# Kernel tuning notes

Hardware: AMD Instinct MI355X
Metric: run time of the kernel (lower is better)

The kernel has to match this reference:

```python
import jax, jax.numpy as jnp
import numpy as np

D = 1024
H = 16
DH = D // H


def setup_inputs() -> dict:
    key = jax.random.key(0)
    ks = jax.random.split(key, 9)
    s = 1.0 / np.sqrt(D)
    return {
        "x": jax.random.normal(ks[0], (4, 2048, D), dtype=jnp.float32),
        "wq": jax.random.uniform(ks[1], (D, D), jnp.float32, -s, s),
        "bq": jax.random.uniform(ks[2], (D,), jnp.float32, -s, s),
        "wk": jax.random.uniform(ks[3], (D, D), jnp.float32, -s, s),
        "bk": jax.random.uniform(ks[4], (D,), jnp.float32, -s, s),
        "wv": jax.random.uniform(ks[5], (D, D), jnp.float32, -s, s),
        "bv": jax.random.uniform(ks[6], (D,), jnp.float32, -s, s),
        "wo": jax.random.uniform(ks[7], (D, D), jnp.float32, -s, s),
        "bo": jax.random.uniform(ks[8], (D,), jnp.float32, -s, s),
    }


def reference(x, wq, bq, wk, bk, wv, bv, wo, bo):
    B, S, _ = x.shape
    # projections + split heads: [B, S, D] -> [B, H, S, Dh]
    def split(t):
        return t.reshape(B, S, H, DH).transpose(0, 2, 1, 3)
    q = split(x @ wq + bq)
    k = split(x @ wk + bk)
    v = split(x @ wv + bv)
    scale = 1.0 / jnp.sqrt(jnp.float32(DH))
    scores = jnp.einsum("bhqd,bhkd->bhqk", q, k) * scale  # [B,H,S,S]
    att = jax.nn.softmax(scores, axis=-1)
    out = jnp.einsum("bhqk,bhkd->bhqd", att, v)  # [B,H,S,Dh]
    out = out.transpose(0, 2, 1, 3).reshape(B, S, D)
    return out @ wo + bo
```

## Files before the change

kernel.cpp:

```cpp
#include <hip/hip_runtime.h>
#include <stdint.h>

typedef float f32x4 __attribute__((ext_vector_type(4)));
typedef __bf16 bf16x8 __attribute__((ext_vector_type(8)));
typedef unsigned short ushort_t;
typedef ushort_t ushortx8 __attribute__((ext_vector_type(8)));
typedef ushort_t ushortx4 __attribute__((ext_vector_type(4)));

#define DEV static __device__ __forceinline__

DEV ushort_t f2bf(float f) {
  union { float f; uint32_t u; } v; v.f = f;
  uint32_t u = v.u;
  return (ushort_t)((u + 0x7FFFu + ((u >> 16) & 1u)) >> 16);
}

DEV uint32_t pkbf(float a, float b) {
  __bf16 x = (__bf16)a, y = (__bf16)b;
  return (uint32_t)__builtin_bit_cast(unsigned short, x) |
         ((uint32_t)__builtin_bit_cast(unsigned short, y) << 16);
}

DEV void cp16(const void* g, void* l) {
  __builtin_amdgcn_global_load_lds((const __attribute__((address_space(1))) unsigned int*)g,
                                   (__attribute__((address_space(3))) unsigned int*)l,
                                   16, 0, 0);
}

DEV f32x4 mfma16(bf16x8 a, bf16x8 b, f32x4 c) {
  return __builtin_amdgcn_mfma_f32_16x16x32_bf16(a, b, c, 0, 0, 0);
}

__global__ __launch_bounds__(256) void k_prep(
    const float* __restrict__ x, ushort_t* __restrict__ xb,
    const float* __restrict__ wq, const float* __restrict__ wk,
    const float* __restrict__ wv, const float* __restrict__ wo,
    ushort_t* __restrict__ wqkvT, ushort_t* __restrict__ woT) {
  __shared__ float tile[32][33];
  int b = blockIdx.x;
  if (b < 4096) {
    size_t idx = ((size_t)b * 256 + threadIdx.x) * 8;
    const float4* src = (const float4*)(x + idx);
    float4 a = src[0], c = src[1];
    ushortx8 o;
    o[0] = f2bf(a.x); o[1] = f2bf(a.y); o[2] = f2bf(a.z); o[3] = f2bf(a.w);
    o[4] = f2bf(c.x); o[5] = f2bf(c.y); o[6] = f2bf(c.z); o[7] = f2bf(c.w);
    *(ushortx8*)(xb + idx) = o;
  } else {
    int t = b - 4096;
    int which = t >> 10;
    const float* src = (which == 0) ? wq : (which == 1) ? wk : (which == 2) ? wv : wo;
    ushort_t* dst = (which == 0) ? wqkvT
                    : (which == 1) ? wqkvT + 1024 * 1024
                    : (which == 2) ? wqkvT + 2 * 1024 * 1024
                                   : woT;
    int tt = t & 1023;
    int c0 = (tt & 31) * 32, r0 = (tt >> 5) * 32;
    int tx = threadIdx.x & 31, ty = threadIdx.x >> 5;
#pragma unroll
    for (int i = ty; i < 32; i += 8)
      tile[i][tx] = src[(size_t)(r0 + i) * 1024 + c0 + tx];
    __syncthreads();
#pragma unroll
    for (int i = ty; i < 32; i += 8)
      dst[(size_t)(c0 + i) * 1024 + r0 + tx] = f2bf(tile[tx][i]);
  }
}

__global__ __launch_bounds__(512, 2) void k_gemm256(
    const ushort_t* __restrict__ A, const ushort_t* __restrict__ Bt,
    const float* __restrict__ b0, const float* __restrict__ b1,
    const float* __restrict__ b2, ushort_t* __restrict__ qw,
    ushort_t* __restrict__ kw, ushort_t* __restrict__ vtw) {
  extern __shared__ ushort_t lds[];
  ushort_t* As = lds;
  ushort_t* Bs = lds + 32768;
  const int K = 1024, NT = 16;
  int tid = threadIdx.x;
  int w = tid >> 6, lane = tid & 63, l16 = lane & 15, lg = lane >> 4;
  int wr = w >> 2, wc = w & 3;
  int m0 = blockIdx.x * 256, n0 = blockIdx.y * 256;

  const ushort_t* Asrc = A + (size_t)(m0 + w * 8 + (lane >> 3)) * K +
                         (size_t)(((lane & 7) ^ (lane >> 3)) * 8);
  const ushort_t* Bsrc = Bt + (size_t)(n0 + w * 8 + (lane >> 3)) * K +
                         (size_t)(((lane & 7) ^ (lane >> 3)) * 8);

  f32x4 acc[8][4] = {};
  bf16x8 a[4][2], b[4][2];
  const int aRow = wr * 128 + l16, bRow = wc * 64 + l16, rsw = l16 & 7;

#pragma unroll
  for (int s = 0; s < 4; ++s)
    cp16(Asrc + (size_t)s * 64 * K, As + s * 4096 + w * 512);
#pragma unroll
  for (int s = 0; s < 4; ++s)
    cp16(Bsrc + (size_t)s * 64 * K, Bs + s * 4096 + w * 512);
  cp16(Asrc + 64, As + 16384 + w * 512);
  cp16(Asrc + (size_t)65536 + 64, As + 16384 + 4096 + w * 512);
  asm volatile("s_waitcnt vmcnt(2)" ::: "memory");
  __builtin_amdgcn_s_barrier();

  for (int t = 0; t < NT; ++t) {
    int cur = t & 1, nxt = cur ^ 1;
    ushort_t* AsC = As + cur * 16384;
    ushort_t* BsC = Bs + cur * 16384;
    ushort_t* AsN = As + nxt * 16384;
    ushort_t* BsN = Bs + nxt * 16384;
    const ushort_t* An = Asrc + (size_t)(t + 1) * 64;
    const ushort_t* Bn = Bsrc + (size_t)(t + 1) * 64;

#pragma unroll
    for (int i2 = 0; i2 < 4; ++i2)
#pragma unroll
      for (int ks = 0; ks < 2; ++ks)
        a[i2][ks] = *(const bf16x8*)&AsC[(aRow + i2 * 16) * 64 +
                                         (((ks << 2) | lg) ^ rsw) * 8];
#pragma unroll
    for (int j2 = 0; j2 < 2; ++j2)
#pragma unroll
      for (int ks = 0; ks < 2; ++ks)
        b[j2][ks] = *(const bf16x8*)&BsC[(bRow + j2 * 16) * 64 +
                                         (((ks << 2) | lg) ^ rsw) * 8];
    cp16(An + (size_t)2 * 65536, AsN + 2 * 4096 + w * 512);
    cp16(An + (size_t)3 * 65536, AsN + 3 * 4096 + w * 512);
    __builtin_amdgcn_s_barrier();
    asm volatile("s_waitcnt lgkmcnt(0)" ::: "memory");
    __builtin_amdgcn_s_setprio(1);
#pragma unroll
    for (int i2 = 0; i2 < 4; ++i2)
#pragma unroll
      for (int j2 = 0; j2 < 2; ++j2)
#pragma unroll
        for (int ks = 0; ks < 2; ++ks)
          acc[i2][j2] = mfma16(a[i2][ks], b[j2][ks], acc[i2][j2]);
    __builtin_amdgcn_s_setprio(0);
    __builtin_amdgcn_s_barrier();

#pragma unroll
    for (int j2 = 2; j2 < 4; ++j2)
#pragma unroll
      for (int ks = 0; ks < 2; ++ks)
        b[j2][ks] = *(const bf16x8*)&BsC[(bRow + j2 * 16) * 64 +
                                         (((ks << 2) | lg) ^ rsw) * 8];
    cp16(Bn, BsN + w * 512);
    cp16(Bn + (size_t)65536, BsN + 4096 + w * 512);
    __builtin_amdgcn_s_barrier();
    asm volatile("s_waitcnt lgkmcnt(0)" ::: "memory");
    __builtin_amdgcn_s_setprio(1);
#pragma unroll
    for (int i2 = 0; i2 < 4; ++i2)
#pragma unroll
      for (int j2 = 2; j2 < 4; ++j2)
#pragma unroll
        for (int ks = 0; ks < 2; ++ks)
          acc[i2][j2] = mfma16(a[i2][ks], b[j2][ks], acc[i2][j2]);
    __builtin_amdgcn_s_setprio(0);
    __builtin_amdgcn_s_barrier();

#pragma unroll
    for (int i2 = 0; i2 < 4; ++i2)
#pragma unroll
      for (int ks = 0; ks < 2; ++ks)
        a[i2][ks] = *(const bf16x8*)&AsC[(aRow + (4 + i2) * 16) * 64 +
                                         (((ks << 2) | lg) ^ rsw) * 8];
    cp16(Bn + (size_t)2 * 65536, BsN + 2 * 4096 + w * 512);
    cp16(Bn + (size_t)3 * 65536, BsN + 3 * 4096 + w * 512);
    __builtin_amdgcn_s_barrier();
    asm volatile("s_waitcnt lgkmcnt(0)" ::: "memory");
    __builtin_amdgcn_s_setprio(1);
#pragma unroll
    for (int i2 = 0; i2 < 4; ++i2)
#pragma unroll
      for (int j2 = 2; j2 < 4; ++j2)
#pragma unroll
        for (int ks = 0; ks < 2; ++ks)
          acc[4 + i2][j2] = mfma16(a[i2][ks], b[j2][ks], acc[4 + i2][j2]);
    __builtin_amdgcn_s_setprio(0);
    __builtin_amdgcn_s_barrier();

    {
      const ushort_t* A2 = Asrc + (size_t)(t + 2) * 64;
      cp16(A2, AsC + w * 512);
      cp16(A2 + (size_t)65536, AsC + 4096 + w * 512);
    }
    asm volatile("s_waitcnt vmcnt(2)" ::: "memory");
    __builtin_amdgcn_s_barrier();
    __builtin_amdgcn_s_setprio(1);
#pragma unroll
    for (int i2 = 0; i2 < 4; ++i2)
#pragma unroll
      for (int j2 = 0; j2 < 2; ++j2)
#pragma unroll
        for (int ks = 0; ks < 2; ++ks)
          acc[4 + i2][j2] = mfma16(a[i2][ks], b[j2][ks], acc[4 + i2][j2]);
    __builtin_amdgcn_s_setprio(0);
    __builtin_amdgcn_s_barrier();
  }

  const float QSCALE = 0.18033688011112042f;
  int p = blockIdx.x >> 2;
  int cbase = (m0 & 1023) + wr * 128;
  if (p == 2) {
#pragma unroll
    for (int i = 0; i < 8; ++i) {
      int oc = cbase + i * 16 + lg * 4;
      int h = oc >> 6, dh0 = oc & 63;
      float4 bb = *(const float4*)&b2[oc];
#pragma unroll
      for (int j = 0; j < 4; ++j) {
        int tok = n0 + wc * 64 + j * 16 + l16;
        int bi = tok >> 11, tk = tok & 2047;
        size_t vb = ((size_t)((bi * 16 + h) * 64 + dh0)) * 2048 + tk;
        vtw[vb] = f2bf(acc[i][j][0] + bb.x);
        vtw[vb + 2048] = f2bf(acc[i][j][1] + bb.y);
        vtw[vb + 2 * 2048] = f2bf(acc[i][j][2] + bb.z);
        vtw[vb + 3 * 2048] = f2bf(acc[i][j][3] + bb.w);
      }
    }
  } else {
    const float* bias = (p == 0) ? b0 : b1;
    ushort_t* dst = (p == 0) ? qw : kw;
    float qs = (p == 0) ? QSCALE : 1.0f;
#pragma unroll
    for (int i = 0; i < 8; ++i) {
      int oc = cbase + i * 16 + lg * 4;
      int h = oc >> 6, dh0 = oc & 63;
      float4 bb = *(const float4*)&bias[oc];
#pragma unroll
      for (int j = 0; j < 4; ++j) {
        int tok = n0 + wc * 64 + j * 16 + l16;
        size_t base =
            ((size_t)((tok >> 11) * 16 + h) * 2048 + (tok & 2047)) * 64 + dh0;
        ushortx4 pk;
        pk[0] = f2bf((acc[i][j][0] + bb.x) * qs);
        pk[1] = f2bf((acc[i][j][1] + bb.y) * qs);
        pk[2] = f2bf((acc[i][j][2] + bb.z) * qs);
        pk[3] = f2bf((acc[i][j][3] + bb.w) * qs);
        *(ushortx4*)&dst[base] = pk;
      }
    }
  }
}

template <int MODE>
__global__ __launch_bounds__(256, 2) void k_gemm(
    const ushort_t* __restrict__ A, const ushort_t* __restrict__ Bt,
    const float* __restrict__ b0, float* __restrict__ outf) {
  const int K = 1024;
  __shared__ ushort_t As[128 * 32];
  __shared__ ushort_t Bs[128 * 32];
  int tid = threadIdx.x;
  int w = tid >> 6, lane = tid & 63, l16 = lane & 15, lg = lane >> 4;
  int m0 = blockIdx.x * 128, n0 = blockIdx.y * 128;
  int wm = (w >> 1) * 64, wn = (w & 1) * 64;
  f32x4 acc[4][4] = {};

  const ushort_t* Ag = A + (size_t)(m0 + (tid >> 2)) * K + (tid & 3) * 8;
  const ushort_t* Bg = Bt + (size_t)(n0 + (tid >> 2)) * K + (tid & 3) * 8;

  for (int k0 = 0; k0 < K; k0 += 32) {
    cp16(Ag + k0, As + w * 512);
    cp16(Ag + k0 + 64 * K, As + 2048 + w * 512);
    cp16(Bg + k0, Bs + w * 512);
    cp16(Bg + k0 + 64 * K, Bs + 2048 + w * 512);
    __syncthreads();
    bf16x8 af[4], bfr[4];
#pragma unroll
    for (int i = 0; i < 4; ++i)
      af[i] = *(const bf16x8*)&As[(wm + i * 16 + l16) * 32 + lg * 8];
#pragma unroll
    for (int j = 0; j < 4; ++j)
      bfr[j] = *(const bf16x8*)&Bs[(wn + j * 16 + l16) * 32 + lg * 8];
#pragma unroll
    for (int i = 0; i < 4; ++i)
#pragma unroll
      for (int j = 0; j < 4; ++j)
        acc[i][j] = mfma16(af[i], bfr[j], acc[i][j]);
    __syncthreads();
  }

#pragma unroll
  for (int j = 0; j < 4; ++j) {
    int col = n0 + wn + j * 16 + l16;
    float bb = b0[col];
#pragma unroll
    for (int i = 0; i < 4; ++i) {
#pragma unroll
      for (int r = 0; r < 4; ++r) {
        int row = m0 + wm + i * 16 + lg * 4 + r;
        outf[(size_t)row * 1024 + col] = acc[i][j][r] + bb;
      }
    }
  }
}

__global__ __launch_bounds__(512, 2) void k_attn(
    const ushort_t* __restrict__ qg, const ushort_t* __restrict__ kg,
    const ushort_t* __restrict__ vtg, ushort_t* __restrict__ att) {
  __shared__ ushort_t Ks[2][64 * 64];
  __shared__ ushort_t Vs[2][64 * 64];
  __shared__ ushort_t Ps[8][16 * 128];
  int tid = threadIdx.x;
  int w = tid >> 6, lane = tid & 63, l16 = lane & 15, lg = lane >> 4;
  int i = blockIdx.x;
  int bh = (i & 7) * 8 + ((i >> 3) & 7);
  int q0 = (i >> 6) * 256;
  const ushort_t* qh = qg + (size_t)bh * 2048 * 64;

  const ushort_t* kstage = kg + (size_t)bh * 2048 * 64 + (size_t)(tid >> 3) * 64 +
                           (size_t)(((tid & 7) ^ ((tid >> 3) & 7)) * 8);
  const ushort_t* vstage = vtg + (size_t)bh * 64 * 2048 + (size_t)(tid >> 3) * 2048 +
                           (size_t)(((tid & 7) ^ ((tid >> 3) & 7)) * 8);

  bf16x8 qf[2][2];
#pragma unroll
  for (int st = 0; st < 2; ++st)
#pragma unroll
    for (int ks = 0; ks < 2; ++ks)
      qf[st][ks] = *(const bf16x8*)(qh + (size_t)(q0 + w * 32 + st * 16 + l16) * 64 +
                                    ks * 32 + lg * 8);

  bf16x8 vone;
#pragma unroll
  for (int t = 0; t < 8; ++t) vone[t] = (__bf16)1.0f;

  f32x4 o[2][5] = {};

  cp16(kstage, &Ks[0][tid * 8]);
  cp16(vstage, &Vs[0][tid * 8]);
  __syncthreads();

  for (int t = 0; t < 32; ++t) {
    int cur = t & 1, nxt = cur ^ 1;
    cp16(kstage + (size_t)(t + 1) * 64 * 64, &Ks[nxt][tid * 8]);
    cp16(vstage + (size_t)(t + 1) * 64, &Vs[nxt][tid * 8]);

    f32x4 sc[2][4] = {};
    __builtin_amdgcn_s_setprio(1);
#pragma unroll
    for (int jt = 0; jt < 4; ++jt) {
      int row = jt * 16 + l16;
      bf16x8 kf0 = *(const bf16x8*)&Ks[cur][row * 64 + ((lg) ^ (l16 & 7)) * 8];
      bf16x8 kf1 = *(const bf16x8*)&Ks[cur][row * 64 + ((lg + 4) ^ (l16 & 7)) * 8];
      sc[0][jt] = mfma16(kf0, qf[0][0], sc[0][jt]);
      sc[0][jt] = mfma16(kf1, qf[0][1], sc[0][jt]);
      sc[1][jt] = mfma16(kf0, qf[1][0], sc[1][jt]);
      sc[1][jt] = mfma16(kf1, qf[1][1], sc[1][jt]);
    }
    __builtin_amdgcn_s_setprio(0);

#pragma unroll
    for (int st = 0; st < 2; ++st)
#pragma unroll
      for (int jt = 0; jt < 4; ++jt) {
        float e0 = __builtin_amdgcn_exp2f(sc[st][jt][0]);
        float e1 = __builtin_amdgcn_exp2f(sc[st][jt][1]);
        float e2 = __builtin_amdgcn_exp2f(sc[st][jt][2]);
        float e3 = __builtin_amdgcn_exp2f(sc[st][jt][3]);
        uint2 pk2;
        pk2.x = pkbf(e0, e1);
        pk2.y = pkbf(e2, e3);
        *(uint2*)&Ps[w][l16 * 128 +
                        (((st * 8 + jt * 2 + (lg >> 1)) ^ l16) * 8) +
                        (lg & 1) * 4] = pk2;
      }

    __builtin_amdgcn_s_setprio(1);
#pragma unroll
    for (int ks = 0; ks < 2; ++ks) {
      bf16x8 pf0 =
          *(const bf16x8*)&Ps[w][l16 * 128 + (((ks * 4 + lg) ^ l16) * 8)];
      bf16x8 pf1 =
          *(const bf16x8*)&Ps[w][l16 * 128 + (((8 + ks * 4 + lg) ^ l16) * 8)];
      o[0][4] = mfma16(pf0, vone, o[0][4]);
      o[1][4] = mfma16(pf1, vone, o[1][4]);
#pragma unroll
      for (int dt = 0; dt < 4; ++dt) {
        int vrow = dt * 16 + l16;
        bf16x8 vf =
            *(const bf16x8*)&Vs[cur][vrow * 64 + (((ks * 4 + lg) ^ (l16 & 7)) * 8)];
        o[0][dt] = mfma16(pf0, vf, o[0][dt]);
        o[1][dt] = mfma16(pf1, vf, o[1][dt]);
      }
    }
    __builtin_amdgcn_s_setprio(0);

    __syncthreads();
  }

  int bi = bh >> 4, h = bh & 15;
#pragma unroll
  for (int st = 0; st < 2; ++st) {
    f32x4 inv;
#pragma unroll
    for (int r = 0; r < 4; ++r) inv[r] = __builtin_amdgcn_rcpf(o[st][4][r]);
#pragma unroll
    for (int dt = 0; dt < 4; ++dt)
#pragma unroll
      for (int r = 0; r < 4; ++r) {
        int srow = q0 + w * 32 + st * 16 + lg * 4 + r;
        int col = h * 64 + dt * 16 + l16;
        att[(size_t)(bi * 2048 + srow) * 1024 + col] = f2bf(o[st][dt][r] * inv[r]);
      }
  }
}

extern "C" void kernel_launch(void* const* d_in, const int* in_sizes, int n_in,
                              void* d_out, int out_size, void* d_ws, size_t ws_size,
                              hipStream_t stream) {
  const float* x = (const float*)d_in[0];
  const float* wq = (const float*)d_in[1];
  const float* bq = (const float*)d_in[2];
  const float* wk = (const float*)d_in[3];
  const float* bk = (const float*)d_in[4];
  const float* wv = (const float*)d_in[5];
  const float* bv = (const float*)d_in[6];
  const float* wo = (const float*)d_in[7];
  const float* bo = (const float*)d_in[8];
  float* out = (float*)d_out;

  char* ws = (char*)d_ws;
  ushort_t* xb = (ushort_t*)(ws);
  ushort_t* wqkvT = (ushort_t*)(ws + 16777216);
  ushort_t* woT = (ushort_t*)(ws + 23068672);
  ushort_t* qw = (ushort_t*)(ws + 25165824);
  ushort_t* kw = (ushort_t*)(ws + 41943040);
  ushort_t* vtw = (ushort_t*)(ws + 58720256);
  ushort_t* att = (ushort_t*)(ws + 75497472);

  k_prep<<<dim3(8192), dim3(256), 0, stream>>>(x, xb, wq, wk, wv, wo, wqkvT, woT);

  const int GEMM0_LDS = 131072;
  hipFuncSetAttribute(reinterpret_cast<const void*>(&k_gemm256),
                      hipFuncAttributeMaxDynamicSharedMemorySize, GEMM0_LDS);
  k_gemm256<<<dim3(12, 32), dim3(512), GEMM0_LDS, stream>>>(
      wqkvT, xb, bq, bk, bv, qw, kw, vtw);

  k_attn<<<dim3(512), dim3(512), 0, stream>>>(qw, kw, vtw, att);

  k_gemm<1><<<dim3(64, 8), dim3(256), 0, stream>>>(att, woT, bo, out);
}
```

Before: 270.4 us.

## Replace output projection GEMM with pipelined 128x256 swizzled-LDS kernel

Replaces the simple 128x128 output-projection GEMM, which synchronises twice per 32-wide K step, with a 512-thread 128x256 tile kernel. The new kernel uses a 64-wide K step, XOR-swizzled LDS layout, and double-buffered global-to-LDS loads interleaved with MFMA phases, plus s_setprio. The aim is to hide load latency, avoid LDS bank conflicts and raise arithmetic intensity. The grid shrinks to 256 blocks at one block per CU, which may underfill the device, and the hand-placed waitcnt/barrier logic is fragile.

After: 273.2 us. Within noise of the previous version (+1.0%).

```diff
diff --git a/kernel.cpp b/kernel.cpp
--- a/kernel.cpp
+++ b/kernel.cpp
@@ -243,52 +243,138 @@
   }
 }
 
-template <int MODE>
-__global__ __launch_bounds__(256, 2) void k_gemm(
+__global__ __launch_bounds__(512, 1) void k_oproj(
     const ushort_t* __restrict__ A, const ushort_t* __restrict__ Bt,
-    const float* __restrict__ b0, float* __restrict__ outf) {
-  const int K = 1024;
-  __shared__ ushort_t As[128 * 32];
-  __shared__ ushort_t Bs[128 * 32];
+    const float* __restrict__ bo, float* __restrict__ outf) {
+  extern __shared__ ushort_t lds[];
+  ushort_t* As2 = lds;
+  ushort_t* Bs2 = lds + 2 * 8192;
+  const int K = 1024, NT = 16;
   int tid = threadIdx.x;
   int w = tid >> 6, lane = tid & 63, l16 = lane & 15, lg = lane >> 4;
-  int m0 = blockIdx.x * 128, n0 = blockIdx.y * 128;
-  int wm = (w >> 1) * 64, wn = (w & 1) * 64;
+  int wr = w >> 2, wc = w & 3;
+  int m0 = blockIdx.x * 128, n0 = blockIdx.y * 256;
+
+  const ushort_t* Asrc = A + (size_t)(m0 + (tid >> 3)) * K +
+                         (size_t)(((tid & 7) ^ ((tid >> 3) & 7)) * 8);
+  const ushort_t* Bsrc = Bt + (size_t)(n0 + (tid >> 3)) * K +
+                         (size_t)(((tid & 7) ^ ((tid >> 3) & 7)) * 8);
+
   f32x4 acc[4][4] = {};
-
-  const ushort_t* Ag = A + (size_t)(m0 + (tid >> 2)) * K + (tid & 3) * 8;
-  const ushort_t* Bg = Bt + (size_t)(n0 + (tid >> 2)) * K + (tid & 3) * 8;
-
-  for (int k0 = 0; k0 < K; k0 += 32) {
-    cp16(Ag + k0, As + w * 512);
-    cp16(Ag + k0 + 64 * K, As + 2048 + w * 512);
-    cp16(Bg + k0, Bs + w * 512);
-    cp16(Bg + k0 + 64 * K, Bs + 2048 + w * 512);
-    __syncthreads();
-    bf16x8 af[4], bfr[4];
-#pragma unroll
-    for (int i = 0; i < 4; ++i)
-      af[i] = *(const bf16x8*)&As[(wm + i * 16 + l16) * 32 + lg * 8];
-#pragma unroll
-    for (int j = 0; j < 4; ++j)
-      bfr[j] = *(const bf16x8*)&Bs[(wn + j * 16 + l16) * 32 + lg * 8];
-#pragma unroll
-    for (int i = 0; i < 4; ++i)
-#pragma unroll
-      for (int j = 0; j < 4; ++j)
-        acc[i][j] = mfma16(af[i], bfr[j], acc[i][j]);
-    __syncthreads();
+  bf16x8 a[2][2], b[4][2];
+  const int aRow = wr * 64 + l16, bRow = wc * 64 + l16, rsw = l16 & 7;
+
+  cp16(Asrc, As2 + w * 512);
+  cp16(Asrc + (size_t)64 * K, As2 + 4096 + w * 512);
+#pragma unroll
+  for (int s = 0; s < 4; ++s)
+    cp16(Bsrc + (size_t)s * 64 * K, Bs2 + s * 4096 + w * 512);
+  cp16(Bsrc + 64, Bs2 + 16384 + w * 512);
+  cp16(Bsrc + 64 + (size_t)64 * K, Bs2 + 16384 + 4096 + w * 512);
+  asm volatile("s_waitcnt vmcnt(2)" ::: "memory");
+  __builtin_amdgcn_s_barrier();
+
+  for (int t = 0; t < NT; ++t) {
+    int cur = t & 1, nxt = cur ^ 1;
+    ushort_t* AsC = As2 + cur * 8192;
+    ushort_t* BsC = Bs2 + cur * 16384;
+    int t1 = (t + 1 < NT) ? t + 1 : NT - 1;
+    int t2 = (t + 2 < NT) ? t + 2 : NT - 1;
+    const ushort_t* An = Asrc + (size_t)t1 * 64;
+    const ushort_t* Bn = Bsrc + (size_t)t1 * 64;
+
+#pragma unroll
+    for (int i2 = 0; i2 < 2; ++i2)
+#pragma unroll
+      for (int ks = 0; ks < 2; ++ks)
+        a[i2][ks] = *(const bf16x8*)&AsC[(aRow + i2 * 16) * 64 +
+                                         (((ks << 2) | lg) ^ rsw) * 8];
+#pragma unroll
+    for (int j2 = 0; j2 < 2; ++j2)
+#pragma unroll
+      for (int ks = 0; ks < 2; ++ks)
+        b[j2][ks] = *(const bf16x8*)&BsC[(bRow + j2 * 16) * 64 +
+                                         (((ks << 2) | lg) ^ rsw) * 8];
+    cp16(Bn + (size_t)2 * 64 * K, Bs2 + nxt * 16384 + 2 * 4096 + w * 512);
+    cp16(Bn + (size_t)3 * 64 * K, Bs2 + nxt * 16384 + 3 * 4096 + w * 512);
+    __builtin_amdgcn_s_barrier();
+    asm volatile("s_waitcnt lgkmcnt(0)" ::: "memory");
+    __builtin_amdgcn_s_setprio(1);
+#pragma unroll
+    for (int i2 = 0; i2 < 2; ++i2)
+#pragma unroll
+      for (int j2 = 0; j2 < 2; ++j2)
+#pragma unroll
+        for (int ks = 0; ks < 2; ++ks)
+          acc[i2][j2] = mfma16(a[i2][ks], b[j2][ks], acc[i2][j2]);
+    __builtin_amdgcn_s_setprio(0);
+    __builtin_amdgcn_s_barrier();
+
+#pragma unroll
+    for (int j2 = 2; j2 < 4; ++j2)
+#pragma unroll
+      for (int ks = 0; ks < 2; ++ks)
+        b[j2][ks] = *(const bf16x8*)&BsC[(bRow + j2 * 16) * 64 +
+                                         (((ks << 2) | lg) ^ rsw) * 8];
+    cp16(An, As2 + nxt * 8192 + w * 512);
+    cp16(An + (size_t)64 * K, As2 + nxt * 8192 + 4096 + w * 512);
+    __builtin_amdgcn_s_barrier();
+    asm volatile("s_waitcnt lgkmcnt(0)" ::: "memory");
+    __builtin_amdgcn_s_setprio(1);
+#pragma unroll
+    for (int i2 = 0; i2 < 2; ++i2)
+#pragma unroll
+      for (int j2 = 2; j2 < 4; ++j2)
+#pragma unroll
+        for (int ks = 0; ks < 2; ++ks)
+          acc[i2][j2] = mfma16(a[i2][ks], b[j2][ks], acc[i2][j2]);
+    __builtin_amdgcn_s_setprio(0);
+    __builtin_amdgcn_s_barrier();
+
+#pragma unroll
+    for (int i2 = 0; i2 < 2; ++i2)
+#pragma unroll
+      for (int ks = 0; ks < 2; ++ks)
+        a[i2][ks] = *(const bf16x8*)&AsC[(aRow + (2 + i2) * 16) * 64 +
+                                         (((ks << 2) | lg) ^ rsw) * 8];
+    __builtin_amdgcn_s_barrier();
+    asm volatile("s_waitcnt lgkmcnt(0)" ::: "memory");
+    __builtin_amdgcn_s_setprio(1);
+#pragma unroll
+    for (int i2 = 0; i2 < 2; ++i2)
+#pragma unroll
+      for (int j2 = 2; j2 < 4; ++j2)
+#pragma unroll
+        for (int ks = 0; ks < 2; ++ks)
+          acc[2 + i2][j2] = mfma16(a[i2][ks], b[j2][ks], acc[2 + i2][j2]);
+    __builtin_amdgcn_s_setprio(0);
+    __builtin_amdgcn_s_barrier();
+
+    cp16(Bsrc + (size_t)t2 * 64, BsC + w * 512);
+    cp16(Bsrc + (size_t)t2 * 64 + (size_t)64 * K, BsC + 4096 + w * 512);
+    asm volatile("s_waitcnt vmcnt(2)" ::: "memory");
+    __builtin_amdgcn_s_barrier();
+    __builtin_amdgcn_s_setprio(1);
+#pragma unroll
+    for (int i2 = 0; i2 < 2; ++i2)
+#pragma unroll
+      for (int j2 = 0; j2 < 2; ++j2)
+#pragma unroll
+        for (int ks = 0; ks < 2; ++ks)
+          acc[2 + i2][j2] = mfma16(a[i2][ks], b[j2][ks], acc[2 + i2][j2]);
+    __builtin_amdgcn_s_setprio(0);
+    __builtin_amdgcn_s_barrier();
   }
 
 #pragma unroll
   for (int j = 0; j < 4; ++j) {
-    int col = n0 + wn + j * 16 + l16;
-    float bb = b0[col];
+    int col = n0 + wc * 64 + j * 16 + l16;
+    float bb = bo[col];
 #pragma unroll
     for (int i = 0; i < 4; ++i) {
 #pragma unroll
       for (int r = 0; r < 4; ++r) {
-        int row = m0 + wm + i * 16 + lg * 4 + r;
+        int row = m0 + wr * 64 + i * 16 + lg * 4 + r;
         outf[(size_t)row * 1024 + col] = acc[i][j][r] + bb;
       }
     }
@@ -439,5 +525,8 @@
 
   k_attn<<<dim3(512), dim3(512), 0, stream>>>(qw, kw, vtw, att);
 
-  k_gemm<1><<<dim3(64, 8), dim3(256), 0, stream>>>(att, woT, bo, out);
-}
+  const int OP_LDS = 98304;
+  hipFuncSetAttribute(reinterpret_cast<const void*>(&k_oproj),
+                      hipFuncAttributeMaxDynamicSharedMemorySize, OP_LDS);
+  k_oproj<<<dim3(64, 4), dim3(512), OP_LDS, stream>>>(att, woT, bo, out);
+}
```

## Replace QKV and output GEMMs with shared 128x256 pipelined kernel template

Applied to the files above, without the earlier changes.

The 256x256 QKV projection kernel is cut to 128x256 tiles, doubling the grid from 384 to 768 blocks. The output projection moves off a simple 128x128 kernel with a barrier-heavy loop onto the same software-pipelined, swizzled, double-buffered template. The aim is better CU occupancy and load balance for QKV, and better latency hiding and reuse for the output GEMM. In exchange QKV does more redundant B-operand traffic per FLOP, and launch_bounds drops to one block per CU.

Result: no change. 270.4 us (+0.0%).

```diff
diff --git a/kernel.cpp b/kernel.cpp
--- a/kernel.cpp
+++ b/kernel.cpp
@@ -67,51 +67,52 @@
   }
 }
 
-__global__ __launch_bounds__(512, 2) void k_gemm256(
+template <int MODE>
+__global__ __launch_bounds__(512, 1) void k_gemm2(
     const ushort_t* __restrict__ A, const ushort_t* __restrict__ Bt,
     const float* __restrict__ b0, const float* __restrict__ b1,
     const float* __restrict__ b2, ushort_t* __restrict__ qw,
-    ushort_t* __restrict__ kw, ushort_t* __restrict__ vtw) {
+    ushort_t* __restrict__ kw, ushort_t* __restrict__ vtw,
+    float* __restrict__ outf) {
   extern __shared__ ushort_t lds[];
-  ushort_t* As = lds;
-  ushort_t* Bs = lds + 32768;
+  ushort_t* As2 = lds;
+  ushort_t* Bs2 = lds + 2 * 8192;
   const int K = 1024, NT = 16;
   int tid = threadIdx.x;
   int w = tid >> 6, lane = tid & 63, l16 = lane & 15, lg = lane >> 4;
   int wr = w >> 2, wc = w & 3;
-  int m0 = blockIdx.x * 256, n0 = blockIdx.y * 256;
-
-  const ushort_t* Asrc = A + (size_t)(m0 + w * 8 + (lane >> 3)) * K +
-                         (size_t)(((lane & 7) ^ (lane >> 3)) * 8);
-  const ushort_t* Bsrc = Bt + (size_t)(n0 + w * 8 + (lane >> 3)) * K +
-                         (size_t)(((lane & 7) ^ (lane >> 3)) * 8);
-
-  f32x4 acc[8][4] = {};
-  bf16x8 a[4][2], b[4][2];
-  const int aRow = wr * 128 + l16, bRow = wc * 64 + l16, rsw = l16 & 7;
-
+  int m0 = blockIdx.x * 128, n0 = blockIdx.y * 256;
+
+  const ushort_t* Asrc = A + (size_t)(m0 + (tid >> 3)) * K +
+                         (size_t)(((tid & 7) ^ ((tid >> 3) & 7)) * 8);
+  const ushort_t* Bsrc = Bt + (size_t)(n0 + (tid >> 3)) * K +
+                         (size_t)(((tid & 7) ^ ((tid >> 3) & 7)) * 8);
+
+  f32x4 acc[4][4] = {};
+  bf16x8 a[2][2], b[4][2];
+  const int aRow = wr * 64 + l16, bRow = wc * 64 + l16, rsw = l16 & 7;
+
+  cp16(Asrc, As2 + w * 512);
+  cp16(Asrc + (size_t)64 * K, As2 + 4096 + w * 512);
 #pragma unroll
   for (int s = 0; s < 4; ++s)
-    cp16(Asrc + (size_t)s * 64 * K, As + s * 4096 + w * 512);
-#pragma unroll
-  for (int s = 0; s < 4; ++s)
-    cp16(Bsrc + (size_t)s * 64 * K, Bs + s * 4096 + w * 512);
-  cp16(Asrc + 64, As + 16384 + w * 512);
-  cp16(Asrc + (size_t)65536 + 64, As + 16384 + 4096 + w * 512);
+    cp16(Bsrc + (size_t)s * 64 * K, Bs2 + s * 4096 + w * 512);
+  cp16(Bsrc + 64, Bs2 + 16384 + w * 512);
+  cp16(Bsrc + 64 + (size_t)64 * K, Bs2 + 16384 + 4096 + w * 512);
   asm volatile("s_waitcnt vmcnt(2)" ::: "memory");
   __builtin_amdgcn_s_barrier();
 
   for (int t = 0; t < NT; ++t) {
     int cur = t & 1, nxt = cur ^ 1;
-    ushort_t* AsC = As + cur * 16384;
-    ushort_t* BsC = Bs + cur * 16384;
-    ushort_t* AsN = As + nxt * 16384;
-    ushort_t* BsN = Bs + nxt * 16384;
-    const ushort_t* An = Asrc + (size_t)(t + 1) * 64;
-    const ushort_t* Bn = Bsrc + (size_t)(t + 1) * 64;
-
-#pragma unroll
-    for (int i2 = 0; i2 < 4; ++i2)
+    ushort_t* AsC = As2 + cur * 8192;
+    ushort_t* BsC = Bs2 + cur * 16384;
+    int t1 = (t + 1 < NT) ? t + 1 : NT - 1;
+    int t2 = (t + 2 < NT) ? t + 2 : NT - 1;
+    const ushort_t* An = Asrc + (size_t)t1 * 64;
+    const ushort_t* Bn = Bsrc + (size_t)t1 * 64;
+
+#pragma unroll
+    for (int i2 = 0; i2 < 2; ++i2)
 #pragma unroll
       for (int ks = 0; ks < 2; ++ks)
         a[i2][ks] = *(const bf16x8*)&AsC[(aRow + i2 * 16) * 64 +
@@ -122,13 +123,13 @@
       for (int ks = 0; ks < 2; ++ks)
         b[j2][ks] = *(const bf16x8*)&BsC[(bRow + j2 * 16) * 64 +
                                          (((ks << 2) | lg) ^ rsw) * 8];
-    cp16(An + (size_t)2 * 65536, AsN + 2 * 4096 + w * 512);
-    cp16(An + (size_t)3 * 65536, AsN + 3 * 4096 + w * 512);
+    cp16(Bn + (size_t)2 * 64 * K, Bs2 + nxt * 16384 + 2 * 4096 + w * 512);
+    cp16(Bn + (size_t)3 * 64 * K, Bs2 + nxt * 16384 + 3 * 4096 + w * 512);
     __builtin_amdgcn_s_barrier();
     asm volatile("s_waitcnt lgkmcnt(0)" ::: "memory");
     __builtin_amdgcn_s_setprio(1);
 #pragma unroll
-    for (int i2 = 0; i2 < 4; ++i2)
+    for (int i2 = 0; i2 < 2; ++i2)
 #pragma unroll
       for (int j2 = 0; j2 < 2; ++j2)
 #pragma unroll
@@ -143,13 +144,13 @@
       for (int ks = 0; ks < 2; ++ks)
         b[j2][ks] = *(const bf16x8*)&BsC[(bRow + j2 * 16) * 64 +
                                          (((ks << 2) | lg) ^ rsw) * 8];
-    cp16(Bn, BsN + w * 512);
-    cp16(Bn + (size_t)65536, BsN + 4096 + w * 512);
+    cp16(An, As2 + nxt * 8192 + w * 512);
+    cp16(An + (size_t)64 * K, As2 + nxt * 8192 + 4096 + w * 512);
     __builtin_amdgcn_s_barrier();
     asm volatile("s_waitcnt lgkmcnt(0)" ::: "memory");
     __builtin_amdgcn_s_setprio(1);
 #pragma unroll
-    for (int i2 = 0; i2 < 4; ++i2)
+    for (int i2 = 0; i2 < 2; ++i2)
 #pragma unroll
       for (int j2 = 2; j2 < 4; ++j2)
 #pragma unroll
@@ -159,137 +160,96 @@
     __builtin_amdgcn_s_barrier();
 
 #pragma unroll
-    for (int i2 = 0; i2 < 4; ++i2)
+    for (int i2 = 0; i2 < 2; ++i2)
 #pragma unroll
       for (int ks = 0; ks < 2; ++ks)
-        a[i2][ks] = *(const bf16x8*)&AsC[(aRow + (4 + i2) * 16) * 64 +
+        a[i2][ks] = *(const bf16x8*)&AsC[(aRow + (2 + i2) * 16) * 64 +
                                          (((ks << 2) | lg) ^ rsw) * 8];
-    cp16(Bn + (size_t)2 * 65536, BsN + 2 * 4096 + w * 512);
-    cp16(Bn + (size_t)3 * 65536, BsN + 3 * 4096 + w * 512);
     __builtin_amdgcn_s_barrier();
     asm volatile("s_waitcnt lgkmcnt(0)" ::: "memory");
     __builtin_amdgcn_s_setprio(1);
 #pragma unroll
-    for (int i2 = 0; i2 < 4; ++i2)
+    for (int i2 = 0; i2 < 2; ++i2)
 #pragma unroll
       for (int j2 = 2; j2 < 4; ++j2)
 #pragma unroll
         for (int ks = 0; ks < 2; ++ks)
-          acc[4 + i2][j2] = mfma16(a[i2][ks], b[j2][ks], acc[4 + i2][j2]);
-    __builtin_amdgcn_s_setprio(0);
-    __builtin_amdgcn_s_barrier();
-
-    {
-      const ushort_t* A2 = Asrc + (size_t)(t + 2) * 64;
-      cp16(A2, AsC + w * 512);
-      cp16(A2 + (size_t)65536, AsC + 4096 + w * 512);
-    }
+          acc[2 + i2][j2] = mfma16(a[i2][ks], b[j2][ks], acc[2 + i2][j2]);
+    __builtin_amdgcn_s_setprio(0);
+    __builtin_amdgcn_s_barrier();
+
+    cp16(Bsrc + (size_t)t2 * 64, BsC + w * 512);
+    cp16(Bsrc + (size_t)t2 * 64 + (size_t)64 * K, BsC + 4096 + w * 512);
     asm volatile("s_waitcnt vmcnt(2)" ::: "memory");
     __builtin_amdgcn_s_barrier();
     __builtin_amdgcn_s_setprio(1);
 #pragma unroll
-    for (int i2 = 0; i2 < 4; ++i2)
+    for (int i2 = 0; i2 < 2; ++i2)
 #pragma unroll
       for (int j2 = 0; j2 < 2; ++j2)
 #pragma unroll
         for (int ks = 0; ks < 2; ++ks)
-          acc[4 + i2][j2] = mfma16(a[i2][ks], b[j2][ks], acc[4 + i2][j2]);
+          acc[2 + i2][j2] = mfma16(a[i2][ks], b[j2][ks], acc[2 + i2][j2]);
     __builtin_amdgcn_s_setprio(0);
     __builtin_amdgcn_s_barrier();
   }
 
-  const float QSCALE = 0.18033688011112042f;
-  int p = blockIdx.x >> 2;
-  int cbase = (m0 & 1023) + wr * 128;
-  if (p == 2) {
-#pragma unroll
-    for (int i = 0; i < 8; ++i) {
-      int oc = cbase + i * 16 + lg * 4;
-      int h = oc >> 6, dh0 = oc & 63;
-      float4 bb = *(const float4*)&b2[oc];
-#pragma unroll
-      for (int j = 0; j < 4; ++j) {
-        int tok = n0 + wc * 64 + j * 16 + l16;
-        int bi = tok >> 11, tk = tok & 2047;
-        size_t vb = ((size_t)((bi * 16 + h) * 64 + dh0)) * 2048 + tk;
-        vtw[vb] = f2bf(acc[i][j][0] + bb.x);
-        vtw[vb + 2048] = f2bf(acc[i][j][1] + bb.y);
-        vtw[vb + 2 * 2048] = f2bf(acc[i][j][2] + bb.z);
-        vtw[vb + 3 * 2048] = f2bf(acc[i][j][3] + bb.w);
+  if (MODE == 0) {
+    const float QSCALE = 0.18033688011112042f;
+    int p = blockIdx.x >> 3;
+    int cbase = (m0 & 1023) + wr * 64;
+    if (p == 2) {
+#pragma unroll
+      for (int i = 0; i < 4; ++i) {
+        int oc = cbase + i * 16 + lg * 4;
+        int h = oc >> 6, dh0 = oc & 63;
+        float4 bb = *(const float4*)&b2[oc];
+#pragma unroll
+        for (int j = 0; j < 4; ++j) {
+          int tok = n0 + wc * 64 + j * 16 + l16;
+          int bi = tok >> 11, tk = tok & 2047;
+          size_t vb = ((size_t)((bi * 16 + h) * 64 + dh0)) * 2048 + tk;
+          vtw[vb] = f2bf(acc[i][j][0] + bb.x);
+          vtw[vb + 2048] = f2bf(acc[i][j][1] + bb.y);
+          vtw[vb + 2 * 2048] = f2bf(acc[i][j][2] + bb.z);
+          vtw[vb + 3 * 2048] = f2bf(acc[i][j][3] + bb.w);
+        }
+      }
+    } else {
+      const float* bias = (p == 0) ? b0 : b1;
+      ushort_t* dst = (p == 0) ? qw : kw;
+      float qs = (p == 0) ? QSCALE : 1.0f;
+#pragma unroll
+      for (int i = 0; i < 4; ++i) {
+        int oc = cbase + i * 16 + lg * 4;
+        int h = oc >> 6, dh0 = oc & 63;
+        float4 bb = *(const float4*)&bias[oc];
+#pragma unroll
+        for (int j = 0; j < 4; ++j) {
+          int tok = n0 + wc * 64 + j * 16 + l16;
+          size_t base =
+              ((size_t)((tok >> 11) * 16 + h) * 2048 + (tok & 2047)) * 64 + dh0;
+          ushortx4 pk;
+          pk[0] = f2bf((acc[i][j][0] + bb.x) * qs);
+          pk[1] = f2bf((acc[i][j][1] + bb.y) * qs);
+          pk[2] = f2bf((acc[i][j][2] + bb.z) * qs);
+          pk[3] = f2bf((acc[i][j][3] + bb.w) * qs);
+          *(ushortx4*)&dst[base] = pk;
+        }
       }
     }
   } else {
-    const float* bias = (p == 0) ? b0 : b1;
-    ushort_t* dst = (p == 0) ? qw : kw;
-    float qs = (p == 0) ? QSCALE : 1.0f;
-#pragma unroll
-    for (int i = 0; i < 8; ++i) {
-      int oc = cbase + i * 16 + lg * 4;
-      int h = oc >> 6, dh0 = oc & 63;
-      float4 bb = *(const float4*)&bias[oc];
-#pragma unroll
-      for (int j = 0; j < 4; ++j) {
-        int tok = n0 + wc * 64 + j * 16 + l16;
-        size_t base =
-            ((size_t)((tok >> 11) * 16 + h) * 2048 + (tok & 2047)) * 64 + dh0;
-        ushortx4 pk;
-        pk[0] = f2bf((acc[i][j][0] + bb.x) * qs);
-        pk[1] = f2bf((acc[i][j][1] + bb.y) * qs);
-        pk[2] = f2bf((acc[i][j][2] + bb.z) * qs);
-        pk[3] = f2bf((acc[i][j][3] + bb.w) * qs);
-        *(ushortx4*)&dst[base] = pk;
-      }
-    }
-  }
-}
-
-template <int MODE>
-__global__ __launch_bounds__(256, 2) void k_gemm(
-    const ushort_t* __restrict__ A, const ushort_t* __restrict__ Bt,
-    const float* __restrict__ b0, float* __restrict__ outf) {
-  const int K = 1024;
-  __shared__ ushort_t As[128 * 32];
-  __shared__ ushort_t Bs[128 * 32];
-  int tid = threadIdx.x;
-  int w = tid >> 6, lane = tid & 63, l16 = lane & 15, lg = lane >> 4;
-  int m0 = blockIdx.x * 128, n0 = blockIdx.y * 128;
-  int wm = (w >> 1) * 64, wn = (w & 1) * 64;
-  f32x4 acc[4][4] = {};
-
-  const ushort_t* Ag = A + (size_t)(m0 + (tid >> 2)) * K + (tid & 3) * 8;
-  const ushort_t* Bg = Bt + (size_t)(n0 + (tid >> 2)) * K + (tid & 3) * 8;
-
-  for (int k0 = 0; k0 < K; k0 += 32) {
-    cp16(Ag + k0, As + w * 512);
-    cp16(Ag + k0 + 64 * K, As + 2048 + w * 512);
-    cp16(Bg + k0, Bs + w * 512);
-    cp16(Bg + k0 + 64 * K, Bs + 2048 + w * 512);
-    __syncthreads();
-    bf16x8 af[4], bfr[4];
-#pragma unroll
-    for (int i = 0; i < 4; ++i)
-      af[i] = *(const bf16x8*)&As[(wm + i * 16 + l16) * 32 + lg * 8];
-#pragma unroll
-    for (int j = 0; j < 4; ++j)
-      bfr[j] = *(const bf16x8*)&Bs[(wn + j * 16 + l16) * 32 + lg * 8];
-#pragma unroll
-    for (int i = 0; i < 4; ++i)
-#pragma unroll
-      for (int j = 0; j < 4; ++j)
-        acc[i][j] = mfma16(af[i], bfr[j], acc[i][j]);
-    __syncthreads();
-  }
-
-#pragma unroll
-  for (int j = 0; j < 4; ++j) {
-    int col = n0 + wn + j * 16 + l16;
-    float bb = b0[col];
-#pragma unroll
-    for (int i = 0; i < 4; ++i) {
-#pragma unroll
-      for (int r = 0; r < 4; ++r) {
-        int row = m0 + wm + i * 16 + lg * 4 + r;
-        outf[(size_t)row * 1024 + col] = acc[i][j][r] + bb;
+#pragma unroll
+    for (int j = 0; j < 4; ++j) {
+      int col = n0 + wc * 64 + j * 16 + l16;
+      float bb = b0[col];
+#pragma unroll
+      for (int i = 0; i < 4; ++i) {
+#pragma unroll
+        for (int r = 0; r < 4; ++r) {
+          int row = m0 + wr * 64 + i * 16 + lg * 4 + r;
+          outf[(size_t)row * 1024 + col] = acc[i][j][r] + bb;
+        }
       }
     }
   }
@@ -431,13 +391,17 @@
 
   k_prep<<<dim3(8192), dim3(256), 0, stream>>>(x, xb, wq, wk, wv, wo, wqkvT, woT);
 
-  const int GEMM0_LDS = 131072;
-  hipFuncSetAttribute(reinterpret_cast<const void*>(&k_gemm256),
-                      hipFuncAttributeMaxDynamicSharedMemorySize, GEMM0_LDS);
-  k_gemm256<<<dim3(12, 32), dim3(512), GEMM0_LDS, stream>>>(
-      wqkvT, xb, bq, bk, bv, qw, kw, vtw);
+  const int G2_LDS = 98304;
+  hipFuncSetAttribute(reinterpret_cast<const void*>(&k_gemm2<0>),
+                      hipFuncAttributeMaxDynamicSharedMemorySize, G2_LDS);
+  hipFuncSetAttribute(reinterpret_cast<const void*>(&k_gemm2<1>),
+                      hipFuncAttributeMaxDynamicSharedMemorySize, G2_LDS);
+
+  k_gemm2<0><<<dim3(24, 32), dim3(512), G2_LDS, stream>>>(
+      wqkvT, xb, bq, bk, bv, qw, kw, vtw, nullptr);
 
   k_attn<<<dim3(512), dim3(512), 0, stream>>>(qw, kw, vtw, att);
 
-  k_gemm<1><<<dim3(64, 8), dim3(256), 0, stream>>>(att, woT, bo, out);
-}
+  k_gemm2<1><<<dim3(64, 4), dim3(512), G2_LDS, stream>>>(
+      att, woT, bo, nullptr, nullptr, nullptr, nullptr, nullptr, out);
+}
```
